# Kernel tuning notes

Measured on AMD Instinct MI355X. Metric: run time of the kernel, lower is better.

The kernel has to match this reference:

```python
import jax, jax.numpy as jnp
import numpy as np

N = 320   # coalition size (number of prefix steps)
D = 512   # input_dim / attention weight_dim


def setup_inputs() -> dict:
    key = jax.random.key(0)
    ks = jax.random.split(key, 10)
    s = 1.0 / np.sqrt(D)  # torch Linear default init range
    u = lambda k, shape: jax.random.uniform(k, shape, jnp.float32, -s, s)
    return {
        "x": jax.random.normal(ks[0], (N, D), jnp.float32),
        "goal": jax.random.normal(ks[1], (D,), jnp.float32),
        "Wq": u(ks[2], (D, D)), "bq": u(ks[3], (D,)),
        "Wk": u(ks[4], (D, D)), "bk": u(ks[5], (D,)),
        "Wv": u(ks[6], (D, D)), "bv": u(ks[7], (D,)),
        # norm_col_init(std=0.1): small column-normalized weights; bias zero-filled
        "Wc": 0.01 * jax.random.normal(ks[8], (1, 2 * D), jnp.float32),
        "bc": jnp.zeros((1,), jnp.float32),
    }


def reference(x, goal, Wq, bq, Wk, bk, Wv, bv, Wc, bc):
    # x: [n, d] coalition features. goal is unused by the original forward.
    n, d = x.shape
    q = x @ Wq.T + bq  # [n, d]
    k = x @ Wk.T + bk
    v = x @ Wv.T + bv
    scores = (q @ k.T) / jnp.sqrt(jnp.asarray(d, x.dtype))  # [n, n]

    # Prefix lengths j = 1..n-1. For each j, attention over coalition[:j]:
    # softmax over keys < j (rows < j are the only valid queries), then the
    # AttentionLayer global feature = mean over query rows of attn @ v.
    j = jnp.arange(1, n)                          # [n-1]
    idx = jnp.arange(n)
    prefix_mask = idx[None, :] < j[:, None]       # [n-1, n], True for k < j
    neg = jnp.finfo(scores.dtype).min
    masked = jnp.where(prefix_mask[:, None, :], scores[None, :, :], neg)  # [n-1, n, n]
    att = jax.nn.softmax(masked, axis=-1)         # rows >= j are garbage, masked below
    # mean over valid query rows i < j, fused before multiplying by V:
    pooled = jnp.sum(att * prefix_mask[:, :, None], axis=1) / j[:, None].astype(x.dtype)  # [n-1, n]
    feats = pooled @ v                            # [n-1, d] global feature per prefix

    # j = 0 uses a zero feature vector
    features = jnp.concatenate([jnp.zeros((1, d), x.dtype), feats], axis=0)  # [n, d]
    cat = jnp.concatenate([features, x], axis=1)  # [n, 2d]
    vals = cat @ Wc.T + bc                        # [n, 1] critic outputs
    return jnp.sum(vals)[None]                    # scalar value, shape [1]
```

## Files before the change

kernel.cpp:

```cpp
#include <hip/hip_runtime.h>

#define NC 320
#define DIM 512

__global__ __launch_bounds__(256) void big1(
    const float* __restrict__ x,
    const float* __restrict__ Wq, const float* __restrict__ Wk,
    const float* __restrict__ Wv, const float* __restrict__ Wc,
    float* __restrict__ partQK,
    float* __restrict__ hpart)
{
  const int b = blockIdx.x;
  const int t = threadIdx.x;

  if (b >= 640) {
    const int d0 = (b - 640) * 32;
    for (int ei = t; ei < DIM; ei += 256) {
      float s = 0.f;
      #pragma unroll
      for (int d = 0; d < 32; ++d)
        s = fmaf(Wv[(d0 + d) * DIM + ei], Wc[d0 + d], s);
      hpart[(b - 640) * DIM + ei] = s;
    }
    return;
  }

  __shared__ __align__(16) float As[32][68];
  __shared__ __align__(16) float Bs[32][68];

  const int z   = b / 40;
  const int rem = b % 40;
  const int i0  = (rem / 8) * 64;
  const int c0  = (rem % 8) * 64;
  const float* __restrict__ W = (z & 8) ? Wk : Wq;
  const int kb = (z & 7) * 64;

  const int sr = t >> 2;
  const int kc = (t & 3) << 3;
  const int ty = t >> 4;
  const int tx = t & 15;

  float acc[4][4] = {};
  const float* xp = x + (i0 + sr) * DIM + kc;
  const float* wp = W + (c0 + sr) * DIM + kc;

  for (int k0 = kb; k0 < kb + 64; k0 += 32) {
    const float4 xa = *(const float4*)(xp + k0);
    const float4 xb = *(const float4*)(xp + k0 + 4);
    const float4 wa = *(const float4*)(wp + k0);
    const float4 wb = *(const float4*)(wp + k0 + 4);
    __syncthreads();
    As[kc+0][sr]=xa.x; As[kc+1][sr]=xa.y; As[kc+2][sr]=xa.z; As[kc+3][sr]=xa.w;
    As[kc+4][sr]=xb.x; As[kc+5][sr]=xb.y; As[kc+6][sr]=xb.z; As[kc+7][sr]=xb.w;
    Bs[kc+0][sr]=wa.x; Bs[kc+1][sr]=wa.y; Bs[kc+2][sr]=wa.z; Bs[kc+3][sr]=wa.w;
    Bs[kc+4][sr]=wb.x; Bs[kc+5][sr]=wb.y; Bs[kc+6][sr]=wb.z; Bs[kc+7][sr]=wb.w;
    __syncthreads();
    #pragma unroll
    for (int kk = 0; kk < 32; ++kk) {
      const float4 a4 = *(const float4*)&As[kk][ty * 4];
      const float4 b4 = *(const float4*)&Bs[kk][tx * 4];
      const float a[4] = {a4.x, a4.y, a4.z, a4.w};
      const float bb[4] = {b4.x, b4.y, b4.z, b4.w};
      #pragma unroll
      for (int i = 0; i < 4; ++i)
        #pragma unroll
        for (int j = 0; j < 4; ++j)
          acc[i][j] = fmaf(a[i], bb[j], acc[i][j]);
    }
  }
  float* outq = partQK + (size_t)z * NC * DIM;
  #pragma unroll
  for (int i = 0; i < 4; ++i) {
    float4 o = {acc[i][0], acc[i][1], acc[i][2], acc[i][3]};
    *(float4*)&outq[(i0 + ty*4 + i) * DIM + c0 + tx*4] = o;
  }
}

__global__ __launch_bounds__(256) void reduce_qk(
    const float* __restrict__ part,
    const float* __restrict__ bq, const float* __restrict__ bk,
    float* __restrict__ q, float* __restrict__ k)
{
  const int mat = blockIdx.y;
  const int f   = blockIdx.x * 256 + threadIdx.x;
  const int row = f >> 7;
  const int col = (f & 127) * 4;
  const float* bias = mat ? bk : bq;
  float4 s = *(const float4*)&bias[col];
  const size_t off = (size_t)row * DIM + col;
  #pragma unroll
  for (int sp = 0; sp < 8; ++sp) {
    const float4 p = *(const float4*)&part[(size_t)(mat*8+sp) * NC * DIM + off];
    s.x += p.x; s.y += p.y; s.z += p.z; s.w += p.w;
  }
  float* out = mat ? k : q;
  *(float4*)&out[off] = s;
}

__global__ __launch_bounds__(256) void scores_u(
    const float* __restrict__ qbuf, const float* __restrict__ kbuf,
    const float* __restrict__ x,    const float* __restrict__ hpart,
    const float* __restrict__ bv,   const float* __restrict__ Wc,
    const float* __restrict__ bc,
    float* __restrict__ partS,
    float* __restrict__ u, float* __restrict__ out)
{
  const int b    = blockIdx.x;
  const int t    = threadIdx.x;
  const int lane = t & 63;
  const int wave = t >> 6;

  if (b >= 200) {
    __shared__ float red[12];
    const int r = b - 200;

    float cp = bv[t] * Wc[t] + bv[t + 256] * Wc[t + 256];
    float su = 0.f, sw = 0.f;
    for (int ei = t; ei < DIM; ei += 256) {
      float hs = 0.f;
      #pragma unroll
      for (int sp = 0; sp < 16; ++sp) hs += hpart[sp * DIM + ei];
      const float xv = x[r * DIM + ei];
      su = fmaf(xv, hs, su);
      sw = fmaf(xv, Wc[DIM + ei], sw);
    }
    #pragma unroll
    for (int off = 32; off; off >>= 1) {
      cp += __shfl_down(cp, off);
      su += __shfl_down(su, off);
      sw += __shfl_down(sw, off);
    }
    if (lane == 0) { red[wave] = cp; red[4 + wave] = su; red[8 + wave] = sw; }
    __syncthreads();
    if (t == 0) {
      const float c  = red[0] + red[1] + red[2] + red[3];
      const float sU = red[4] + red[5] + red[6] + red[7];
      float sW = red[8] + red[9] + red[10] + red[11];
      u[r] = sU + c;
      if (r == 0) sW += (float)NC * bc[0];
      atomicAdd(out, sW);
    }
    return;
  }

  __shared__ __align__(16) float As[32][68];
  __shared__ __align__(16) float Bs[32][68];

  const int z   = b / 25;
  const int rem = b % 25;
  const int i0  = (rem / 5) * 64;
  const int j0  = (rem % 5) * 64;
  const int kb  = z * 64;

  const int sr = t >> 2;
  const int kc = (t & 3) << 3;
  const int ty = t >> 4;
  const int tx = t & 15;

  float acc[4][4] = {};
  const float* qp = qbuf + (i0 + sr) * DIM + kc;
  const float* kp = kbuf + (j0 + sr) * DIM + kc;

  for (int k0 = kb; k0 < kb + 64; k0 += 32) {
    const float4 qa  = *(const float4*)(qp + k0);
    const float4 qb2 = *(const float4*)(qp + k0 + 4);
    const float4 ka  = *(const float4*)(kp + k0);
    const float4 kb4 = *(const float4*)(kp + k0 + 4);
    __syncthreads();
    As[kc+0][sr]=qa.x;  As[kc+1][sr]=qa.y;  As[kc+2][sr]=qa.z;  As[kc+3][sr]=qa.w;
    As[kc+4][sr]=qb2.x; As[kc+5][sr]=qb2.y; As[kc+6][sr]=qb2.z; As[kc+7][sr]=qb2.w;
    Bs[kc+0][sr]=ka.x;  Bs[kc+1][sr]=ka.y;  Bs[kc+2][sr]=ka.z;  Bs[kc+3][sr]=ka.w;
    Bs[kc+4][sr]=kb4.x; Bs[kc+5][sr]=kb4.y; Bs[kc+6][sr]=kb4.z; Bs[kc+7][sr]=kb4.w;
    __syncthreads();
    #pragma unroll
    for (int kk = 0; kk < 32; ++kk) {
      const float4 a4 = *(const float4*)&As[kk][ty * 4];
      const float4 b4 = *(const float4*)&Bs[kk][tx * 4];
      const float a[4] = {a4.x, a4.y, a4.z, a4.w};
      const float bb[4] = {b4.x, b4.y, b4.z, b4.w};
      #pragma unroll
      for (int i = 0; i < 4; ++i)
        #pragma unroll
        for (int j = 0; j < 4; ++j)
          acc[i][j] = fmaf(a[i], bb[j], acc[i][j]);
    }
  }
  float* outs = partS + (size_t)z * NC * NC;
  #pragma unroll
  for (int i = 0; i < 4; ++i) {
    float4 o = {acc[i][0], acc[i][1], acc[i][2], acc[i][3]};
    *(float4*)&outs[(i0 + ty*4 + i) * NC + j0 + tx*4] = o;
  }
}

__global__ __launch_bounds__(256) void row_ops3(
    const float* __restrict__ partS, const float* __restrict__ u,
    float* __restrict__ out)
{
  const int i    = blockIdx.x;
  const int t    = threadIdx.x;
  const int lane = t & 63;
  const int wave = t >> 6;

  __shared__ float e[NC];
  __shared__ float Warr[NC];
  __shared__ float Csuf[NC + 1];
  __shared__ float wred[4];

  const float scale = 0.044194173824159216f;
  for (int kk = t; kk < NC; kk += 256) {
    float s = 0.f;
    #pragma unroll
    for (int sp = 0; sp < 8; ++sp)
      s += partS[(size_t)sp * NC * NC + i * NC + kk];
    e[kk] = s * scale;
  }
  __syncthreads();

  float m = -1e30f;
  for (int kk = t; kk < NC; kk += 256) m = fmaxf(m, e[kk]);
  #pragma unroll
  for (int off = 32; off; off >>= 1) m = fmaxf(m, __shfl_down(m, off));
  if (lane == 0) wred[wave] = m;
  __syncthreads();
  m = fmaxf(fmaxf(wred[0], wred[1]), fmaxf(wred[2], wred[3]));

  for (int kk = t; kk < NC; kk += 256) e[kk] = __expf(e[kk] - m);
  __syncthreads();

  if (wave == 0) {
    float carry = 0.f;
    #pragma unroll
    for (int c = 0; c < 5; ++c) {
      const int idx = c * 64 + lane;
      float val = e[idx];
      #pragma unroll
      for (int off = 1; off < 64; off <<= 1) {
        const float nv = __shfl_up(val, off);
        if (lane >= off) val += nv;
      }
      const float incl = val + carry;
      const int j = idx + 1;
      if (j < NC) Warr[j] = (j > i) ? 1.f / ((float)j * incl) : 0.f;
      carry += __shfl(val, 63);
    }
    if (lane == 0) Warr[0] = 0.f;

    carry = 0.f;
    #pragma unroll
    for (int c = 4; c >= 0; --c) {
      const int idx = c * 64 + lane;
      float val = Warr[idx];
      #pragma unroll
      for (int off = 1; off < 64; off <<= 1) {
        const float nv = __shfl_down(val, off);
        if (lane + off < 64) val += nv;
      }
      Csuf[idx] = val + carry;
      carry += __shfl(val, 0);
    }
    if (lane == 0) Csuf[NC] = 0.f;
  }
  __syncthreads();

  float acc = 0.f;
  for (int kk = t; kk < NC; kk += 256) {
    const int mm = (i > kk) ? i : kk;
    acc += e[kk] * Csuf[mm + 1] * u[kk];
  }
  #pragma unroll
  for (int off = 32; off; off >>= 1) acc += __shfl_down(acc, off);
  __syncthreads();
  if (lane == 0) wred[wave] = acc;
  __syncthreads();
  if (t == 0)
    atomicAdd(out, wred[0] + wred[1] + wred[2] + wred[3]);
}

extern "C" void kernel_launch(void* const* d_in, const int* in_sizes, int n_in,
                              void* d_out, int out_size, void* d_ws, size_t ws_size,
                              hipStream_t stream) {
  const float* x  = (const float*)d_in[0];
  const float* Wq = (const float*)d_in[2];
  const float* bq = (const float*)d_in[3];
  const float* Wk = (const float*)d_in[4];
  const float* bk = (const float*)d_in[5];
  const float* Wv = (const float*)d_in[6];
  const float* bv = (const float*)d_in[7];
  const float* Wc = (const float*)d_in[8];
  const float* bc = (const float*)d_in[9];

  float* ws     = (float*)d_ws;
  float* partQK = ws;
  float* partS  = partQK + 16 * NC * DIM;
  float* qbuf   = partS + 8 * NC * NC;
  float* kbuf   = qbuf + NC * DIM;
  float* hpart  = kbuf + NC * DIM;
  float* u      = hpart + 16 * DIM;
  float* out    = (float*)d_out;

  hipMemsetAsync(out, 0, sizeof(float), stream);

  big1<<<656, 256, 0, stream>>>(x, Wq, Wk, Wv, Wc, partQK, hpart);
  reduce_qk<<<dim3(160, 2), 256, 0, stream>>>(partQK, bq, bk, qbuf, kbuf);
  scores_u<<<520, 256, 0, stream>>>(qbuf, kbuf, x, hpart, bv, Wc, bc,
                                    partS, u, out);
  row_ops3<<<NC, 256, 0, stream>>>(partS, u, out);
}
```

Measured before the change: 105.1 us.

## Fuse split-K Q/K reduction into score GEMM loads and drop memset

Removes the separate reduce_qk kernel and sums the eight split-K partials plus bias directly while loading Q and K tiles in the score GEMM. The output zeroing moves from a memset into the first GEMM kernel. This cuts two launches and the q/k round trip to memory. In exchange, each score block re-reads and re-reduces partials redundantly across tiles, which raises L2/global read traffic.

Result: slower. 108.0 us (+2.7%).

```diff
diff --git a/kernel.cpp b/kernel.cpp
--- a/kernel.cpp
+++ b/kernel.cpp
@@ -8,12 +8,14 @@
     const float* __restrict__ Wq, const float* __restrict__ Wk,
     const float* __restrict__ Wv, const float* __restrict__ Wc,
     float* __restrict__ partQK,
-    float* __restrict__ hpart)
+    float* __restrict__ hpart,
+    float* __restrict__ out)
 {
   const int b = blockIdx.x;
   const int t = threadIdx.x;
 
   if (b >= 640) {
+    if (b == 640 && t == 0) out[0] = 0.f;
     const int d0 = (b - 640) * 32;
     for (int ei = t; ei < DIM; ei += 256) {
       float s = 0.f;
@@ -76,31 +78,11 @@
   }
 }
 
-__global__ __launch_bounds__(256) void reduce_qk(
-    const float* __restrict__ part,
+__global__ __launch_bounds__(256) void scores_u2(
+    const float* __restrict__ partQK,
     const float* __restrict__ bq, const float* __restrict__ bk,
-    float* __restrict__ q, float* __restrict__ k)
-{
-  const int mat = blockIdx.y;
-  const int f   = blockIdx.x * 256 + threadIdx.x;
-  const int row = f >> 7;
-  const int col = (f & 127) * 4;
-  const float* bias = mat ? bk : bq;
-  float4 s = *(const float4*)&bias[col];
-  const size_t off = (size_t)row * DIM + col;
-  #pragma unroll
-  for (int sp = 0; sp < 8; ++sp) {
-    const float4 p = *(const float4*)&part[(size_t)(mat*8+sp) * NC * DIM + off];
-    s.x += p.x; s.y += p.y; s.z += p.z; s.w += p.w;
-  }
-  float* out = mat ? k : q;
-  *(float4*)&out[off] = s;
-}
-
-__global__ __launch_bounds__(256) void scores_u(
-    const float* __restrict__ qbuf, const float* __restrict__ kbuf,
-    const float* __restrict__ x,    const float* __restrict__ hpart,
-    const float* __restrict__ bv,   const float* __restrict__ Wc,
+    const float* __restrict__ x,  const float* __restrict__ hpart,
+    const float* __restrict__ bv, const float* __restrict__ Wc,
     const float* __restrict__ bc,
     float* __restrict__ partS,
     float* __restrict__ u, float* __restrict__ out)
@@ -158,19 +140,32 @@
   const int tx = t & 15;
 
   float acc[4][4] = {};
-  const float* qp = qbuf + (i0 + sr) * DIM + kc;
-  const float* kp = kbuf + (j0 + sr) * DIM + kc;
 
   for (int k0 = kb; k0 < kb + 64; k0 += 32) {
-    const float4 qa  = *(const float4*)(qp + k0);
-    const float4 qb2 = *(const float4*)(qp + k0 + 4);
-    const float4 ka  = *(const float4*)(kp + k0);
-    const float4 kb4 = *(const float4*)(kp + k0 + 4);
-    __syncthreads();
-    As[kc+0][sr]=qa.x;  As[kc+1][sr]=qa.y;  As[kc+2][sr]=qa.z;  As[kc+3][sr]=qa.w;
-    As[kc+4][sr]=qb2.x; As[kc+5][sr]=qb2.y; As[kc+6][sr]=qb2.z; As[kc+7][sr]=qb2.w;
-    Bs[kc+0][sr]=ka.x;  Bs[kc+1][sr]=ka.y;  Bs[kc+2][sr]=ka.z;  Bs[kc+3][sr]=ka.w;
-    Bs[kc+4][sr]=kb4.x; Bs[kc+5][sr]=kb4.y; Bs[kc+6][sr]=kb4.z; Bs[kc+7][sr]=kb4.w;
+    float4 qa = *(const float4*)&bq[k0 + kc];
+    float4 qb = *(const float4*)&bq[k0 + kc + 4];
+    float4 ka = *(const float4*)&bk[k0 + kc];
+    float4 k2 = *(const float4*)&bk[k0 + kc + 4];
+    const size_t qoff = (size_t)(i0 + sr) * DIM + k0 + kc;
+    const size_t koff = (size_t)(j0 + sr) * DIM + k0 + kc;
+    #pragma unroll
+    for (int sp = 0; sp < 8; ++sp) {
+      const float* pq = partQK + (size_t)sp * (NC * DIM);
+      const float* pk = partQK + (size_t)(8 + sp) * (NC * DIM);
+      const float4 a0 = *(const float4*)(pq + qoff);
+      const float4 a1 = *(const float4*)(pq + qoff + 4);
+      const float4 b0 = *(const float4*)(pk + koff);
+      const float4 b1 = *(const float4*)(pk + koff + 4);
+      qa.x += a0.x; qa.y += a0.y; qa.z += a0.z; qa.w += a0.w;
+      qb.x += a1.x; qb.y += a1.y; qb.z += a1.z; qb.w += a1.w;
+      ka.x += b0.x; ka.y += b0.y; ka.z += b0.z; ka.w += b0.w;
+      k2.x += b1.x; k2.y += b1.y; k2.z += b1.z; k2.w += b1.w;
+    }
+    __syncthreads();
+    As[kc+0][sr]=qa.x; As[kc+1][sr]=qa.y; As[kc+2][sr]=qa.z; As[kc+3][sr]=qa.w;
+    As[kc+4][sr]=qb.x; As[kc+5][sr]=qb.y; As[kc+6][sr]=qb.z; As[kc+7][sr]=qb.w;
+    Bs[kc+0][sr]=ka.x; Bs[kc+1][sr]=ka.y; Bs[kc+2][sr]=ka.z; Bs[kc+3][sr]=ka.w;
+    Bs[kc+4][sr]=k2.x; Bs[kc+5][sr]=k2.y; Bs[kc+6][sr]=k2.z; Bs[kc+7][sr]=k2.w;
     __syncthreads();
     #pragma unroll
     for (int kk = 0; kk < 32; ++kk) {
@@ -293,17 +288,12 @@
   float* ws     = (float*)d_ws;
   float* partQK = ws;
   float* partS  = partQK + 16 * NC * DIM;
-  float* qbuf   = partS + 8 * NC * NC;
-  float* kbuf   = qbuf + NC * DIM;
-  float* hpart  = kbuf + NC * DIM;
+  float* hpart  = partS + 8 * NC * NC;
   float* u      = hpart + 16 * DIM;
   float* out    = (float*)d_out;
 
-  hipMemsetAsync(out, 0, sizeof(float), stream);
-
-  big1<<<656, 256, 0, stream>>>(x, Wq, Wk, Wv, Wc, partQK, hpart);
-  reduce_qk<<<dim3(160, 2), 256, 0, stream>>>(partQK, bq, bk, qbuf, kbuf);
-  scores_u<<<520, 256, 0, stream>>>(qbuf, kbuf, x, hpart, bv, Wc, bc,
-                                    partS, u, out);
+  big1<<<656, 256, 0, stream>>>(x, Wq, Wk, Wv, Wc, partQK, hpart, out);
+  scores_u2<<<520, 256, 0, stream>>>(partQK, bq, bk, x, hpart, bv, Wc, bc,
+                                     partS, u, out);
   row_ops3<<<NC, 256, 0, stream>>>(partS, u, out);
 }
```
